# Performance work log

Measured on AMD Instinct MI355X. Metric: run time of the kernel, lower is better.

Reference implementation:

```python
import jax, jax.numpy as jnp
import numpy as np

EMBED_DIM = 384
HIDDEN_DIM = 512
CODEBOOK_SIZE = 256
NUM_QUANTIZERS = 4
COMMIT_WEIGHT = 0.25
BATCH = 65536


def setup_inputs() -> dict:
    key = jax.random.key(0)
    ks = jax.random.split(key, 10)
    s_in = 1.0 / np.sqrt(EMBED_DIM)
    s_h = 1.0 / np.sqrt(HIDDEN_DIM)
    return {
        "x": jax.random.normal(ks[0], (BATCH, EMBED_DIM), jnp.float32),
        "enc_w1": jax.random.uniform(ks[1], (EMBED_DIM, HIDDEN_DIM), jnp.float32, -s_in, s_in),
        "enc_b1": jnp.zeros((HIDDEN_DIM,), jnp.float32),
        "enc_w2": jax.random.uniform(ks[2], (HIDDEN_DIM, HIDDEN_DIM), jnp.float32, -s_h, s_h),
        "enc_b2": jnp.zeros((HIDDEN_DIM,), jnp.float32),
        "codebooks": jax.random.normal(ks[3], (NUM_QUANTIZERS, CODEBOOK_SIZE, HIDDEN_DIM), jnp.float32),
        "dec_w1": jax.random.uniform(ks[4], (HIDDEN_DIM, HIDDEN_DIM), jnp.float32, -s_h, s_h),
        "dec_b1": jnp.zeros((HIDDEN_DIM,), jnp.float32),
        "dec_w2": jax.random.uniform(ks[5], (HIDDEN_DIM, EMBED_DIM), jnp.float32, -s_h, s_h),
        "dec_b2": jnp.zeros((EMBED_DIM,), jnp.float32),
    }


def _residual_vq(z, codebooks):
    """Sequential residual VQ with straight-through estimator and commitment loss.
    z: [B, D]; codebooks: [Q, K, D]. Returns quantized [B, D], indices [B, Q], commit_loss scalar."""
    residual = z
    quantized_out = jnp.zeros_like(z)
    commit_loss = jnp.asarray(0.0, z.dtype)
    idx_list = []
    for q in range(NUM_QUANTIZERS):
        cb = codebooks[q]  # [K, D]
        # nearest code: argmin ||r - c||^2 == argmax (2 r.c - ||c||^2)
        scores = 2.0 * (residual @ cb.T) - jnp.sum(cb * cb, axis=-1)  # [B, K]
        idx = jnp.argmax(scores, axis=-1)  # [B]
        quant = cb[idx]  # [B, D] gather
        commit_loss = commit_loss + COMMIT_WEIGHT * jnp.mean(
            (residual - jax.lax.stop_gradient(quant)) ** 2)
        # straight-through: value = quant, gradient flows to residual
        quant_st = residual + jax.lax.stop_gradient(quant - residual)
        quantized_out = quantized_out + quant_st
        residual = residual - jax.lax.stop_gradient(quant)
        idx_list.append(idx)
    indices = jnp.stack(idx_list, axis=-1)  # [B, Q]
    return quantized_out, indices, commit_loss


def reference(x, enc_w1, enc_b1, enc_w2, enc_b2, codebooks,
              dec_w1, dec_b1, dec_w2, dec_b2):
    # encoder MLP
    z = jax.nn.relu(x @ enc_w1 + enc_b1) @ enc_w2 + enc_b2  # [B, H]
    quantized, indices, commit_loss = _residual_vq(z, codebooks)
    # decoder MLP
    recon = jax.nn.relu(quantized @ dec_w1 + dec_b1) @ dec_w2 + dec_b2  # [B, E]
    recon_loss = jnp.mean((recon - x) ** 2)
    return recon, indices, recon_loss, commit_loss
```

## Files before the change

### kernel.cpp

```cpp
#include <hip/hip_runtime.h>
#include <cfloat>
#include <cstddef>
#include <cstdint>


#define BATCH   65536
#define EDIM    384
#define HDIM    512
#define NCODE   256
#define NQ      4

#define OUT_IDX_OFF 25165824
#define OUT_RL_OFF  25427968
#define WS_P0       0
#define WS_P1       33554432
#define WS_CBW      67108864
#define WS_CNORM    67633152
#define WS_COMMITP  67634176
#define WS_RECONP   67636224
#define WS_W1S      67637760
#define WS_W2S      67834368
#define WS_W3S      68096512
#define WS_W4S      68358656
#define WS_CBA      68555264
#define WS_G6       69079552
#define WS_ZN       69472768
#define WS_SSTAR    69538304
#define WS_IDXI     69800448

typedef _Float16 half8 __attribute__((ext_vector_type(8)));
typedef float    f32x16 __attribute__((ext_vector_type(16)));

__device__ __forceinline__ void cvt_hl8(const float* vs, half8& h, half8& l)
{
#pragma unroll
    for (int j = 0; j < 8; ++j) {
        _Float16 hv = (_Float16)vs[j];
        h[j] = hv;
        l[j] = (_Float16)(vs[j] - (float)hv);
    }
}

__device__ __forceinline__ void gll16(const unsigned short* g, unsigned short* l)
{
    __builtin_amdgcn_global_load_lds(
        (const __attribute__((address_space(1))) unsigned int*)g,
        (__attribute__((address_space(3))) unsigned int*)l, 16, 0, 0);
}

template <int N> __device__ __forceinline__ void waitvm()
{
    __builtin_amdgcn_sched_barrier(0);
    if constexpr (N == 0)      asm volatile("s_waitcnt vmcnt(0)" ::: "memory");
    else if constexpr (N == 2) asm volatile("s_waitcnt vmcnt(2)" ::: "memory");
    else if constexpr (N == 3) asm volatile("s_waitcnt vmcnt(3)" ::: "memory");
    else if constexpr (N == 4) asm volatile("s_waitcnt vmcnt(4)" ::: "memory");
    else if constexpr (N == 6) asm volatile("s_waitcnt vmcnt(6)" ::: "memory");
    __builtin_amdgcn_sched_barrier(0);
}
__device__ __forceinline__ void barrier_raw()
{
    __builtin_amdgcn_s_barrier();
    __builtin_amdgcn_sched_barrier(0);
}

__global__ __launch_bounds__(256)
void split_act(const float* __restrict__ src, unsigned short* __restrict__ dst,
               int K)
{
    int u = blockIdx.x * 256 + threadIdx.x;
    int upr = K >> 3;
    int row = u / upr;
    int rem = u % upr;
    int kt = rem >> 1, kh = rem & 1;
    const float* p = src + (size_t)row * K + kt * 16 + kh * 8;
    float vs[8];
#pragma unroll
    for (int j = 0; j < 8; ++j) vs[j] = p[j];
    half8 h, l;
    cvt_hl8(vs, h, l);
    unsigned short* o = dst + (size_t)row * (2 * K) + kt * 32 + kh * 8;
    *reinterpret_cast<half8*>(o)      = h;
    *reinterpret_cast<half8*>(o + 16) = l;
}

__device__ __forceinline__ void body_split_w(const float* __restrict__ W,
                                             unsigned short* __restrict__ out,
                                             int N, int u)
{
    int col  = u % N;
    int rem  = u / N;
    int kh   = rem & 1;
    int kt   = rem >> 1;
    int kbase = kt * 16 + kh * 8;
    float vs[8];
#pragma unroll
    for (int j = 0; j < 8; ++j) vs[j] = W[(size_t)(kbase + j) * N + col];
    half8 h, l;
    cvt_hl8(vs, h, l);
    *reinterpret_cast<half8*>(out + ((size_t)(kt * 4 + kh) * N + col) * 8)     = h;
    *reinterpret_cast<half8*>(out + ((size_t)(kt * 4 + 2 + kh) * N + col) * 8) = l;
}

__device__ __forceinline__ void body_split_cbw(const float* __restrict__ cb,
                                               unsigned short* __restrict__ out,
                                               int u)
{
    int col = u & 1023;
    int rem = u >> 10;
    int kh = rem & 1;
    int kt = rem >> 1;
    const float* p = cb + (size_t)col * HDIM + kt * 16 + kh * 8;
    float vs[8];
#pragma unroll
    for (int j = 0; j < 8; ++j) vs[j] = p[j];
    half8 h, l;
    cvt_hl8(vs, h, l);
    *reinterpret_cast<half8*>(out + ((size_t)(kt * 4 + kh) * 1024 + col) * 8)     = h;
    *reinterpret_cast<half8*>(out + ((size_t)(kt * 4 + 2 + kh) * 1024 + col) * 8) = l;
}

__device__ __forceinline__ void body_split_cba(const float* __restrict__ cb,
                                               unsigned short* __restrict__ out,
                                               int u)
{
    int row = u >> 6;
    int rem = u & 63;
    int kt = rem >> 1, kh = rem & 1;
    const float* p = cb + (size_t)row * HDIM + kt * 16 + kh * 8;
    float vs[8];
#pragma unroll
    for (int j = 0; j < 8; ++j) vs[j] = p[j];
    half8 h, l;
    cvt_hl8(vs, h, l);
    unsigned short* o = out + (size_t)row * 1024 + kt * 32 + kh * 8;
    *reinterpret_cast<half8*>(o)      = h;
    *reinterpret_cast<half8*>(o + 16) = l;
}

__global__ __launch_bounds__(256)
void split_wall(const float* __restrict__ ew1, const float* __restrict__ ew2,
                const float* __restrict__ dw1, const float* __restrict__ dw2,
                const float* __restrict__ cb,
                unsigned short* __restrict__ w1s, unsigned short* __restrict__ w2s,
                unsigned short* __restrict__ w3s, unsigned short* __restrict__ w4s,
                unsigned short* __restrict__ cbw, unsigned short* __restrict__ cba)
{
    const int b = blockIdx.x, tid = threadIdx.x;
    if (b < 96)        body_split_w(ew1, w1s, HDIM, b * 256 + tid);
    else if (b < 224)  body_split_w(ew2, w2s, HDIM, (b - 96) * 256 + tid);
    else if (b < 352)  body_split_w(dw1, w3s, HDIM, (b - 224) * 256 + tid);
    else if (b < 448)  body_split_w(dw2, w4s, EDIM, (b - 352) * 256 + tid);
    else if (b < 704)  body_split_cbw(cb, cbw, (b - 448) * 256 + tid);
    else               body_split_cba(cb, cba, (b - 704) * 256 + tid);
}

__global__ __launch_bounds__(64)
void cnorm_kernel(const float* __restrict__ cb, float* __restrict__ cnorm)
{
    const int code = blockIdx.x;
    const int lane = threadIdx.x;
    const float* r = cb + (size_t)code * HDIM;
    float s = 0.f;
    for (int k = lane; k < HDIM; k += 64) s = fmaf(r[k], r[k], s);
#pragma unroll
    for (int off = 32; off > 0; off >>= 1) s += __shfl_down(s, off);
    if (lane == 0) cnorm[code] = s;
}

__global__ __launch_bounds__(256)
void rownorm(const unsigned short* __restrict__ zs, float* __restrict__ zn)
{
    const int tid = threadIdx.x, wid = tid >> 6, lane = tid & 63;
    const int row = blockIdx.x * 4 + wid;
    const unsigned short* p = zs + (size_t)row * 1024
                                 + (lane >> 1) * 32 + (lane & 1) * 8;
    half8 h = *reinterpret_cast<const half8*>(p);
    half8 l = *reinterpret_cast<const half8*>(p + 16);
    float s = 0.f;
#pragma unroll
    for (int e = 0; e < 8; ++e) {
        float v = (float)h[e] + (float)l[e];
        s = fmaf(v, v, s);
    }
#pragma unroll
    for (int off = 32; off > 0; off >>= 1) s += __shfl_down(s, off);
    if (lane == 0) zn[row] = s;
}

template <int BN, int NKT, int OMODE, bool RELU, bool S3, bool OUTH>
__global__ __launch_bounds__(512, 2)
void gemm_pl(const unsigned short* __restrict__ Ain,
             const unsigned short* __restrict__ Wsp,
             const float* __restrict__ bias, void* __restrict__ Cout,
             const float* __restrict__ X, float* __restrict__ lossP,
             int N, int ldc)
{
    constexpr int WN  = BN / 64;
    constexpr int WM  = 8 / WN;
    constexpr int MR  = 256 / WM;
    constexpr int FM  = MR / 32;
    constexpr int K   = NKT * 16;
    constexpr int BOFF = S3 ? 8192 : 4096;
    constexpr int BUFU = BOFF + 32 * BN;
    constexpr int GPI  = (S3 ? 2 : 1) + ((BN == 256) ? 2 : 1);

    __shared__ __align__(16) unsigned short lds[3][BUFU];

    const int tid  = threadIdx.x;
    const int wid  = tid >> 6;
    const int lane = tid & 63;
    const int l31  = lane & 31;
    const int lh   = lane >> 5;
    const int wm   = wid / WN;
    const int wn   = wid % WN;

    int row0, n0, bx = 0, by = 0, pair = 0;
    const unsigned short* Abase = Ain;
    if constexpr (OMODE == 3) {
        const int ptab[6] = {0, 0, 0, 1, 1, 2};
        const int qtab[6] = {1, 2, 3, 2, 3, 3};
        pair = blockIdx.x;
        Abase = Ain + (size_t)ptab[pair] * 256 * 1024;
        row0 = 0;
        n0   = qtab[pair] * 256;
    } else {
        int bidx = blockIdx.y * gridDim.x + blockIdx.x;
        const int nwg = gridDim.x * gridDim.y;
        if ((nwg & 7) == 0) {
            const int cpx = nwg >> 3;
            bidx = (bidx & 7) * cpx + (bidx >> 3);
        }
        bx = bidx % gridDim.x;
        by = bidx / gridDim.x;
        row0 = by * 256;
        n0   = bx * BN;
    }

    f32x16 acc[FM][2];
#pragma unroll
    for (int m = 0; m < FM; ++m)
#pragma unroll
        for (int n = 0; n < 2; ++n) acc[m][n] = (f32x16)(0.0f);

    auto stageA = [&](int buf, int kt) {
#pragma unroll
        for (int t = 0; t < (S3 ? 2 : 1); ++t) {
            const int i = t * 8 + wid;
            const int u = i >> 2;
            const int row = (i & 3) * 64 + lane;
            gll16(Abase + (size_t)(row0 + row) * (2 * K) + kt * 32 + u * 8,
                  &lds[buf][(size_t)i * 512 + (size_t)lane * 8]);
        }
    };
    auto stageB = [&](int buf, int kt) {
        const unsigned short* img = Wsp + (size_t)kt * 4 * N * 8;
        unsigned short* dstb = &lds[buf][BOFF];
        if constexpr (BN == 256) {
#pragma unroll
            for (int t = 0; t < 2; ++t) {
                const int i = t * 8 + wid;
                const int u = i >> 2;
                const int col = (i & 3) * 64 + lane;
                gll16(img + ((size_t)u * N + n0 + col) * 8,
                      dstb + (size_t)i * 512 + (size_t)lane * 8);
            }
        } else {
            const int u = wid >> 1;
            const int col = (wid & 1) * 64 + lane;
            gll16(img + ((size_t)u * N + n0 + col) * 8,
                  dstb + (size_t)wid * 512 + (size_t)lane * 8);
        }
    };
    auto compute = [&](int buf) {
        const unsigned short* Ab = &lds[buf][0];
        const unsigned short* Bb = &lds[buf][BOFF];
        half8 Ah[FM], Al[FM];
#pragma unroll
        for (int fm = 0; fm < FM; ++fm) {
            const int row = wm * MR + fm * 32 + l31;
            Ah[fm] = *reinterpret_cast<const half8*>(Ab + ((size_t)lh * 256 + row) * 8);
            if constexpr (S3)
                Al[fm] = *reinterpret_cast<const half8*>(Ab + ((size_t)(2 + lh) * 256 + row) * 8);
        }
#pragma unroll
        for (int nt = 0; nt < 2; ++nt) {
            const int col = wn * 64 + nt * 32 + l31;
            half8 Bh = *reinterpret_cast<const half8*>(Bb + ((size_t)lh * BN + col) * 8);
            half8 Bl = *reinterpret_cast<const half8*>(Bb + ((size_t)(2 + lh) * BN + col) * 8);
#pragma unroll
            for (int fm = 0; fm < FM; ++fm) {
                acc[fm][nt] = __builtin_amdgcn_mfma_f32_32x32x16_f16(Ah[fm], Bh, acc[fm][nt], 0, 0, 0);
                acc[fm][nt] = __builtin_amdgcn_mfma_f32_32x32x16_f16(Ah[fm], Bl, acc[fm][nt], 0, 0, 0);
                if constexpr (S3)
                    acc[fm][nt] = __builtin_amdgcn_mfma_f32_32x32x16_f16(Al[fm], Bh, acc[fm][nt], 0, 0, 0);
            }
        }
    };

    stageA(0, 0); stageB(0, 0);
    stageA(1, 1); stageB(1, 1);
    waitvm<GPI>();
    barrier_raw();
    for (int kt = 0; kt < NKT; ++kt) {
        const int cur = kt % 3;
        if (kt + 2 < NKT) { const int nb = (kt + 2) % 3; stageA(nb, kt + 2); stageB(nb, kt + 2); }
        compute(cur);
        if (kt < NKT - 2) waitvm<GPI>(); else waitvm<0>();
        barrier_raw();
    }

    if constexpr (OMODE == 0) {
        unsigned short* o = (unsigned short*)Cout;
        const size_t rs = (size_t)N * 2;
#pragma unroll
        for (int fm = 0; fm < FM; ++fm) {
#pragma unroll
            for (int nt = 0; nt < 2; ++nt) {
                const int col = n0 + wn * 64 + nt * 32 + l31;
                const float b = bias[col];
                const size_t cbo = (size_t)(col >> 4) * 32 + (size_t)((col >> 3) & 1) * 8 + (col & 7);
#pragma unroll
                for (int rg = 0; rg < 16; ++rg) {
                    const int row = row0 + wm * MR + fm * 32 + (rg & 3) + 8 * (rg >> 2) + 4 * lh;
                    float v = acc[fm][nt][rg] + b;
                    if (RELU) v = v > 0.f ? v : 0.f;
                    _Float16 hv = (_Float16)v;
                    union { _Float16 f; unsigned short u; } ch;
                    ch.f = hv;
                    o[(size_t)row * rs + cbo] = ch.u;
                    if constexpr (!OUTH) {
                        _Float16 lv = (_Float16)(v - (float)hv);
                        union { _Float16 f; unsigned short u; } cl;
                        cl.f = lv;
                        o[(size_t)row * rs + cbo + 16] = cl.u;
                    }
                }
            }
        }
    } else if constexpr (OMODE == 1) {
        float* C = (float*)Cout;
        float lacc = 0.f;
#pragma unroll
        for (int fm = 0; fm < FM; ++fm) {
#pragma unroll
            for (int nt = 0; nt < 2; ++nt) {
                const int col = n0 + wn * 64 + nt * 32 + l31;
                if (col < N) {
                    const float b = bias[col];
#pragma unroll
                    for (int rg = 0; rg < 16; ++rg) {
                        const int row = row0 + wm * MR + fm * 32 + (rg & 3) + 8 * (rg >> 2) + 4 * lh;
                        float v = acc[fm][nt][rg] + b;
                        if (RELU) v = v > 0.f ? v : 0.f;
                        C[(size_t)row * N + col] = v;
                        float d = v - X[(size_t)row * N + col];
                        lacc = fmaf(d, d, lacc);
                    }
                }
            }
        }
        __shared__ float red[512];
        red[tid] = lacc;
        __syncthreads();
        for (int s = 256; s > 0; s >>= 1) {
            if (tid < s) red[tid] += red[tid + s];
            __syncthreads();
        }
        if (tid == 0) lossP[by * gridDim.x + bx] = red[0];
    } else if constexpr (OMODE == 2) {
        float* C = (float*)Cout;
#pragma unroll
        for (int fm = 0; fm < FM; ++fm) {
#pragma unroll
            for (int nt = 0; nt < 2; ++nt) {
                const int col = n0 + wn * 64 + nt * 32 + l31;
#pragma unroll
                for (int rg = 0; rg < 16; ++rg) {
                    const int row = row0 + wm * MR + fm * 32 + (rg & 3) + 8 * (rg >> 2) + 4 * lh;
                    C[(size_t)row * ldc + col] = acc[fm][nt][rg];
                }
            }
        }
    } else {
        float* C = (float*)Cout + (size_t)pair * 65536;
#pragma unroll
        for (int fm = 0; fm < FM; ++fm) {
#pragma unroll
            for (int nt = 0; nt < 2; ++nt) {
                const int colL = wn * 64 + nt * 32 + l31;
#pragma unroll
                for (int rg = 0; rg < 16; ++rg) {
                    const int row = wm * MR + fm * 32 + (rg & 3) + 8 * (rg >> 2) + 4 * lh;
                    C[(size_t)row * 256 + colL] = acc[fm][nt][rg];
                }
            }
        }
    }
}

__global__ __launch_bounds__(256)
void vq_argmax(const float* __restrict__ S,
               const float* __restrict__ G6,
               const float* __restrict__ cnorm,
               float* __restrict__ idx_out,
               int* __restrict__ idxi,
               float* __restrict__ sstar,
               int rowbase)
{
    const int tid = threadIdx.x, wid = tid >> 6, lane = tid & 63;
    const int lrow = blockIdx.x * 4 + wid;
    const int grow = rowbase + lrow;
    const float* srow = S + (size_t)lrow * 1024;
    const int c0 = lane * 4;

    int iprev0 = 0, iprev1 = 0, iprev2 = 0;

#pragma unroll
    for (int q = 0; q < NQ; ++q) {
        float4 sv = *reinterpret_cast<const float4*>(srow + q * 256 + c0);
        float a[4] = {sv.x, sv.y, sv.z, sv.w};
        if (q >= 1) {
            const float* g = G6 + ((size_t)(q - 1) * 256 + iprev0) * 256 + c0;
            float4 gv = *reinterpret_cast<const float4*>(g);
            a[0] -= gv.x; a[1] -= gv.y; a[2] -= gv.z; a[3] -= gv.w;
        }
        if (q >= 2) {
            const float* g = G6 + ((size_t)(q + 1) * 256 + iprev1) * 256 + c0;
            float4 gv = *reinterpret_cast<const float4*>(g);
            a[0] -= gv.x; a[1] -= gv.y; a[2] -= gv.z; a[3] -= gv.w;
        }
        if (q >= 3) {
            const float* g = G6 + ((size_t)5 * 256 + iprev2) * 256 + c0;
            float4 gv = *reinterpret_cast<const float4*>(g);
            a[0] -= gv.x; a[1] -= gv.y; a[2] -= gv.z; a[3] -= gv.w;
        }
        float4 cnv = *reinterpret_cast<const float4*>(cnorm + q * 256 + c0);
        float cna[4] = {cnv.x, cnv.y, cnv.z, cnv.w};

        float bv = -FLT_MAX;
        int   bi = 0;
#pragma unroll
        for (int j = 0; j < 4; ++j) {
            float s = 2.f * a[j] - cna[j];
            const int code = c0 + j;
            if (s > bv || (s == bv && code < bi)) { bv = s; bi = code; }
        }
#pragma unroll
        for (int m = 1; m < 64; m <<= 1) {
            float ov = __shfl_xor(bv, m, 64);
            int   oi = __shfl_xor(bi, m, 64);
            if (ov > bv || (ov == bv && oi < bi)) { bv = ov; bi = oi; }
        }
        if (q == 0) iprev0 = bi;
        else if (q == 1) iprev1 = bi;
        else if (q == 2) iprev2 = bi;
        if (lane == 0) {
            idxi[q * 65536 + grow]  = bi;
            sstar[q * 65536 + grow] = bv;
            idx_out[(size_t)grow * NQ + q] = (float)bi;
        }
    }
}

__global__ __launch_bounds__(256)
void vq_quant(const int* __restrict__ idxi, const float* __restrict__ sstar,
              const float* __restrict__ zn, const float* __restrict__ cb,
              unsigned short* __restrict__ qout, float* __restrict__ commitP)
{
    __shared__ float red[256];
    const int tid = threadIdx.x, wid = tid >> 6, lane = tid & 63;
    float ca = 0.f;

#pragma unroll
    for (int t = 0; t < 8; ++t) {
        const int row = blockIdx.x * 32 + wid * 8 + t;
        const int i0 = idxi[row],          i1 = idxi[65536 + row];
        const int i2 = idxi[131072 + row], i3 = idxi[196608 + row];
        const int koff = lane * 8;
        const float* c0 = cb + ((size_t)(0 * NCODE + i0)) * HDIM + koff;
        const float* c1 = cb + ((size_t)(1 * NCODE + i1)) * HDIM + koff;
        const float* c2 = cb + ((size_t)(2 * NCODE + i2)) * HDIM + koff;
        const float* c3 = cb + ((size_t)(3 * NCODE + i3)) * HDIM + koff;
        float q[8];
#pragma unroll
        for (int hh = 0; hh < 2; ++hh) {
            float4 v0 = *reinterpret_cast<const float4*>(c0 + hh * 4);
            float4 v1 = *reinterpret_cast<const float4*>(c1 + hh * 4);
            float4 v2 = *reinterpret_cast<const float4*>(c2 + hh * 4);
            float4 v3 = *reinterpret_cast<const float4*>(c3 + hh * 4);
            q[hh * 4 + 0] = ((v0.x + v1.x) + v2.x) + v3.x;
            q[hh * 4 + 1] = ((v0.y + v1.y) + v2.y) + v3.y;
            q[hh * 4 + 2] = ((v0.z + v1.z) + v2.z) + v3.z;
            q[hh * 4 + 3] = ((v0.w + v1.w) + v2.w) + v3.w;
        }
        half8 oh;
#pragma unroll
        for (int e = 0; e < 8; ++e) oh[e] = (_Float16)q[e];
        unsigned short* op = qout + (size_t)row * 1024
                                  + (lane >> 1) * 32 + (lane & 1) * 8;
        *reinterpret_cast<half8*>(op) = oh;

        if (lane == 0) {
            float rn = zn[row];
            rn -= sstar[row];           float cm = rn;
            rn -= sstar[65536 + row];   cm += rn;
            rn -= sstar[131072 + row];  cm += rn;
            rn -= sstar[196608 + row];  cm += rn;
            ca += cm;
        }
    }

    red[tid] = ca;
    __syncthreads();
    for (int s = 128; s > 0; s >>= 1) {
        if (tid < s) red[tid] += red[tid + s];
        __syncthreads();
    }
    if (tid == 0) commitP[blockIdx.x] = red[0];
}

__global__ __launch_bounds__(256)
void loss_reduce(const float* __restrict__ cP, int nc,
                 const float* __restrict__ rP, int nr,
                 float* __restrict__ out2)
{
    __shared__ float red[256];
    const int tid = threadIdx.x;

    float s = 0.f;
    for (int i = tid; i < nc; i += 256) s += cP[i];
    red[tid] = s;
    __syncthreads();
    for (int st = 128; st > 0; st >>= 1) {
        if (tid < st) red[tid] += red[tid + st];
        __syncthreads();
    }
    float ctot = red[0];
    __syncthreads();

    s = 0.f;
    for (int i = tid; i < nr; i += 256) s += rP[i];
    red[tid] = s;
    __syncthreads();
    for (int st = 128; st > 0; st >>= 1) {
        if (tid < st) red[tid] += red[tid + st];
        __syncthreads();
    }
    if (tid == 0) {
        out2[0] = red[0] / ((float)BATCH * (float)EDIM);
        out2[1] = 0.25f * ctot / ((float)BATCH * (float)HDIM);
    }
}

extern "C" void kernel_launch(void* const* d_in, const int* in_sizes, int n_in,
                              void* d_out, int out_size, void* d_ws, size_t ws_size,
                              hipStream_t stream)
{
    const float* x   = (const float*)d_in[0];
    const float* ew1 = (const float*)d_in[1];
    const float* eb1 = (const float*)d_in[2];
    const float* ew2 = (const float*)d_in[3];
    const float* eb2 = (const float*)d_in[4];
    const float* cb  = (const float*)d_in[5];
    const float* dw1 = (const float*)d_in[6];
    const float* db1 = (const float*)d_in[7];
    const float* dw2 = (const float*)d_in[8];
    const float* db2 = (const float*)d_in[9];

    float* out = (float*)d_out;
    float* ws  = (float*)d_ws;
    unsigned short* P0  = (unsigned short*)(ws + WS_P0);
    unsigned short* P1  = (unsigned short*)(ws + WS_P1);
    unsigned short* XS  = P1;
    float* Sbuf = ws + WS_P0;
    unsigned short* cbw = (unsigned short*)(ws + WS_CBW);
    unsigned short* cba = (unsigned short*)(ws + WS_CBA);
    float* G6 = ws + WS_G6;
    float* zn = ws + WS_ZN;
    float* ss = ws + WS_SSTAR;
    int*   ii = (int*)(ws + WS_IDXI);
    float* cn = ws + WS_CNORM;
    float* cP = ws + WS_COMMITP;
    float* rP = ws + WS_RECONP;
    unsigned short* w1s = (unsigned short*)(ws + WS_W1S);
    unsigned short* w2s = (unsigned short*)(ws + WS_W2S);
    unsigned short* w3s = (unsigned short*)(ws + WS_W3S);
    unsigned short* w4s = (unsigned short*)(ws + WS_W4S);

    cnorm_kernel<<<NQ * NCODE, 64, 0, stream>>>(cb, cn);
    split_act<<<BATCH * 48 / 256, 256, 0, stream>>>(x, XS, EDIM);
    split_wall<<<960, 256, 0, stream>>>(ew1, ew2, dw1, dw2, cb,
                                        w1s, w2s, w3s, w4s, cbw, cba);

    gemm_pl<256, 32, 3, false, true, false><<<dim3(6, 1), 512, 0, stream>>>(
        cba, cbw, nullptr, G6, nullptr, nullptr, 1024, 256);

    gemm_pl<256, 24, 0, true, true, false><<<dim3(HDIM / 256, BATCH / 256), 512, 0, stream>>>(
        XS, w1s, eb1, P0, nullptr, nullptr, HDIM, HDIM);
    gemm_pl<256, 32, 0, false, true, false><<<dim3(HDIM / 256, BATCH / 256), 512, 0, stream>>>(
        P0, w2s, eb2, P1, nullptr, nullptr, HDIM, HDIM);

    rownorm<<<BATCH / 4, 256, 0, stream>>>(P1, zn);

    float* idxo = out + OUT_IDX_OFF;
    for (int half = 0; half < 2; ++half) {
        const int rowbase = half * 32768;
        gemm_pl<256, 32, 2, false, true, false><<<dim3(4, 128), 512, 0, stream>>>(
            P1 + (size_t)rowbase * 1024, cbw, nullptr, Sbuf,
            nullptr, nullptr, 1024, 1024);
        vq_argmax<<<8192, 256, 0, stream>>>(Sbuf, G6, cn, idxo, ii, ss, rowbase);
    }

    vq_quant<<<BATCH / 32, 256, 0, stream>>>(ii, ss, zn, cb, P0, cP);

    gemm_pl<256, 32, 0, true, false, true><<<dim3(HDIM / 256, BATCH / 256), 512, 0, stream>>>(
        P0, w3s, db1, P1, nullptr, nullptr, HDIM, HDIM);
    gemm_pl<128, 32, 1, false, false, false><<<dim3(EDIM / 128, BATCH / 256), 512, 0, stream>>>(
        P1, w4s, db2, out, x, rP, EDIM, EDIM);

    loss_reduce<<<1, 256, 0, stream>>>(cP, BATCH / 32, rP,
                                       (EDIM / 128) * (BATCH / 256),
                                       out + OUT_RL_OFF);
}
```

Before: 848.8 us.

## Restructure GEMM LDS pipeline to double-buffer two k-tiles per barrier

Replaces the three-stage single-k-tile ring buffer with a two-buffer scheme where each buffer holds two k-tiles. Each iteration prefetches the next pair while computing two k-tiles, then waits on vmcnt(0) and synchronizes, halving the number of barriers per GEMM. The cost is a full wait on outstanding loads each step rather than partial vmcnt waits, and a larger LDS footprint (four tiles instead of three), which may reduce occupancy and lower prefetch depth relative to compute.

```diff
diff --git a/kernel.cpp b/kernel.cpp
--- a/kernel.cpp
+++ b/kernel.cpp
@@ -48,14 +48,10 @@
         (__attribute__((address_space(3))) unsigned int*)l, 16, 0, 0);
 }
 
-template <int N> __device__ __forceinline__ void waitvm()
+__device__ __forceinline__ void waitvm0()
 {
     __builtin_amdgcn_sched_barrier(0);
-    if constexpr (N == 0)      asm volatile("s_waitcnt vmcnt(0)" ::: "memory");
-    else if constexpr (N == 2) asm volatile("s_waitcnt vmcnt(2)" ::: "memory");
-    else if constexpr (N == 3) asm volatile("s_waitcnt vmcnt(3)" ::: "memory");
-    else if constexpr (N == 4) asm volatile("s_waitcnt vmcnt(4)" ::: "memory");
-    else if constexpr (N == 6) asm volatile("s_waitcnt vmcnt(6)" ::: "memory");
+    asm volatile("s_waitcnt vmcnt(0)" ::: "memory");
     __builtin_amdgcn_sched_barrier(0);
 }
 __device__ __forceinline__ void barrier_raw()
@@ -201,11 +197,11 @@
     constexpr int MR  = 256 / WM;
     constexpr int FM  = MR / 32;
     constexpr int K   = NKT * 16;
-    constexpr int BOFF = S3 ? 8192 : 4096;
-    constexpr int BUFU = BOFF + 32 * BN;
-    constexpr int GPI  = (S3 ? 2 : 1) + ((BN == 256) ? 2 : 1);
-
-    __shared__ __align__(16) unsigned short lds[3][BUFU];
+    constexpr int BOFF  = S3 ? 8192 : 4096;
+    constexpr int TILEU = BOFF + 32 * BN;
+    constexpr int NP    = NKT / 2;
+
+    __shared__ __align__(16) unsigned short lds[2][2 * TILEU];
 
     const int tid  = threadIdx.x;
     const int wid  = tid >> 6;
@@ -243,19 +239,20 @@
 #pragma unroll
         for (int n = 0; n < 2; ++n) acc[m][n] = (f32x16)(0.0f);
 
-    auto stageA = [&](int buf, int kt) {
+    auto stageA = [&](int buf, int slot, int kt) {
+        unsigned short* base = &lds[buf][(size_t)slot * TILEU];
 #pragma unroll
         for (int t = 0; t < (S3 ? 2 : 1); ++t) {
             const int i = t * 8 + wid;
             const int u = i >> 2;
             const int row = (i & 3) * 64 + lane;
             gll16(Abase + (size_t)(row0 + row) * (2 * K) + kt * 32 + u * 8,
-                  &lds[buf][(size_t)i * 512 + (size_t)lane * 8]);
+                  base + (size_t)i * 512 + (size_t)lane * 8);
         }
     };
-    auto stageB = [&](int buf, int kt) {
+    auto stageB = [&](int buf, int slot, int kt) {
         const unsigned short* img = Wsp + (size_t)kt * 4 * N * 8;
-        unsigned short* dstb = &lds[buf][BOFF];
+        unsigned short* dstb = &lds[buf][(size_t)slot * TILEU + BOFF];
         if constexpr (BN == 256) {
 #pragma unroll
             for (int t = 0; t < 2; ++t) {
@@ -272,9 +269,9 @@
                   dstb + (size_t)wid * 512 + (size_t)lane * 8);
         }
     };
-    auto compute = [&](int buf) {
-        const unsigned short* Ab = &lds[buf][0];
-        const unsigned short* Bb = &lds[buf][BOFF];
+    auto compute = [&](int buf, int slot) {
+        const unsigned short* Ab = &lds[buf][(size_t)slot * TILEU];
+        const unsigned short* Bb = Ab + BOFF;
         half8 Ah[FM], Al[FM];
 #pragma unroll
         for (int fm = 0; fm < FM; ++fm) {
@@ -298,15 +295,20 @@
         }
     };
 
-    stageA(0, 0); stageB(0, 0);
-    stageA(1, 1); stageB(1, 1);
-    waitvm<GPI>();
+    stageA(0, 0, 0); stageB(0, 0, 0);
+    stageA(0, 1, 1); stageB(0, 1, 1);
+    waitvm0();
     barrier_raw();
-    for (int kt = 0; kt < NKT; ++kt) {
-        const int cur = kt % 3;
-        if (kt + 2 < NKT) { const int nb = (kt + 2) % 3; stageA(nb, kt + 2); stageB(nb, kt + 2); }
-        compute(cur);
-        if (kt < NKT - 2) waitvm<GPI>(); else waitvm<0>();
+    for (int p = 0; p < NP; ++p) {
+        const int cur = p & 1;
+        if (p + 1 < NP) {
+            const int nb = cur ^ 1;
+            stageA(nb, 0, 2 * p + 2); stageB(nb, 0, 2 * p + 2);
+            stageA(nb, 1, 2 * p + 3); stageB(nb, 1, 2 * p + 3);
+        }
+        compute(cur, 0);
+        compute(cur, 1);
+        waitvm0();
         barrier_raw();
     }
 
```

Measured after the change: 876.6 us. 1.03x slower.

## Add phased double-pair LDS pipeline with setprio for BN=256 split-3 GEMM

Applied to the files above, without the earlier changes.

For the BN=256, three-MFMA split-precision GEMM variant, the kernel now uses four LDS tile slots that hold two k-tile pairs at once. The main loop is split into four phases per pair, and the global-to-LDS loads for the next pair are spread across those phases. Explicit barriers and lgkmcnt waits separate the LDS reads from the MFMA bursts, and s_setprio raises wave priority during the MFMA sections. The aim is to overlap memory traffic with MFMA work better and to reduce contention between waves. In exchange, LDS use grows, which may cut occupancy, and each pair now carries more barriers.

```diff
diff --git a/kernel.cpp b/kernel.cpp
--- a/kernel.cpp
+++ b/kernel.cpp
@@ -58,6 +58,11 @@
     else if constexpr (N == 6) asm volatile("s_waitcnt vmcnt(6)" ::: "memory");
     __builtin_amdgcn_sched_barrier(0);
 }
+__device__ __forceinline__ void waitlgkm0()
+{
+    asm volatile("s_waitcnt lgkmcnt(0)" ::: "memory");
+    __builtin_amdgcn_sched_barrier(0);
+}
 __device__ __forceinline__ void barrier_raw()
 {
     __builtin_amdgcn_s_barrier();
@@ -201,11 +206,13 @@
     constexpr int MR  = 256 / WM;
     constexpr int FM  = MR / 32;
     constexpr int K   = NKT * 16;
-    constexpr int BOFF = S3 ? 8192 : 4096;
-    constexpr int BUFU = BOFF + 32 * BN;
+    constexpr int BOFF  = S3 ? 8192 : 4096;
+    constexpr int TILEU = BOFF + 32 * BN;
+    constexpr bool PHASED = (BN == 256) && S3;
+    constexpr int LDSU = PHASED ? 4 * TILEU : 3 * TILEU;
     constexpr int GPI  = (S3 ? 2 : 1) + ((BN == 256) ? 2 : 1);
 
-    __shared__ __align__(16) unsigned short lds[3][BUFU];
+    __shared__ __align__(16) unsigned short lds[LDSU];
 
     const int tid  = threadIdx.x;
     const int wid  = tid >> 6;
@@ -215,15 +222,15 @@
     const int wm   = wid / WN;
     const int wn   = wid % WN;
 
-    int row0, n0, bx = 0, by = 0, pair = 0;
+    int row0, n0, bx = 0, by = 0, pairi = 0;
     const unsigned short* Abase = Ain;
     if constexpr (OMODE == 3) {
         const int ptab[6] = {0, 0, 0, 1, 1, 2};
         const int qtab[6] = {1, 2, 3, 2, 3, 3};
-        pair = blockIdx.x;
-        Abase = Ain + (size_t)ptab[pair] * 256 * 1024;
+        pairi = blockIdx.x;
+        Abase = Ain + (size_t)ptab[pairi] * 256 * 1024;
         row0 = 0;
-        n0   = qtab[pair] * 256;
+        n0   = qtab[pairi] * 256;
     } else {
         int bidx = blockIdx.y * gridDim.x + blockIdx.x;
         const int nwg = gridDim.x * gridDim.y;
@@ -243,19 +250,20 @@
 #pragma unroll
         for (int n = 0; n < 2; ++n) acc[m][n] = (f32x16)(0.0f);
 
-    auto stageA = [&](int buf, int kt) {
+    auto stageA = [&](int slot, int kt) {
+        unsigned short* base = lds + (size_t)slot * TILEU;
 #pragma unroll
         for (int t = 0; t < (S3 ? 2 : 1); ++t) {
             const int i = t * 8 + wid;
             const int u = i >> 2;
             const int row = (i & 3) * 64 + lane;
             gll16(Abase + (size_t)(row0 + row) * (2 * K) + kt * 32 + u * 8,
-                  &lds[buf][(size_t)i * 512 + (size_t)lane * 8]);
+                  base + (size_t)i * 512 + (size_t)lane * 8);
         }
     };
-    auto stageB = [&](int buf, int kt) {
+    auto stageB = [&](int slot, int kt) {
         const unsigned short* img = Wsp + (size_t)kt * 4 * N * 8;
-        unsigned short* dstb = &lds[buf][BOFF];
+        unsigned short* dstb = lds + (size_t)slot * TILEU + BOFF;
         if constexpr (BN == 256) {
 #pragma unroll
             for (int t = 0; t < 2; ++t) {
@@ -272,9 +280,9 @@
                   dstb + (size_t)wid * 512 + (size_t)lane * 8);
         }
     };
-    auto compute = [&](int buf) {
-        const unsigned short* Ab = &lds[buf][0];
-        const unsigned short* Bb = &lds[buf][BOFF];
+    auto compute = [&](int slot) {
+        const unsigned short* Ab = lds + (size_t)slot * TILEU;
+        const unsigned short* Bb = Ab + BOFF;
         half8 Ah[FM], Al[FM];
 #pragma unroll
         for (int fm = 0; fm < FM; ++fm) {
@@ -298,16 +306,67 @@
         }
     };
 
-    stageA(0, 0); stageB(0, 0);
-    stageA(1, 1); stageB(1, 1);
-    waitvm<GPI>();
-    barrier_raw();
-    for (int kt = 0; kt < NKT; ++kt) {
-        const int cur = kt % 3;
-        if (kt + 2 < NKT) { const int nb = (kt + 2) % 3; stageA(nb, kt + 2); stageB(nb, kt + 2); }
-        compute(cur);
-        if (kt < NKT - 2) waitvm<GPI>(); else waitvm<0>();
+    if constexpr (PHASED) {
+        constexpr int NP = NKT / 2;
+        stageA(0, 0); stageB(0, 0);
+        stageA(1, 1); stageB(1, 1);
+        waitvm<0>();
         barrier_raw();
+        for (int pr = 0; pr < NP; ++pr) {
+            const int cb2 = (pr & 1) * 2;
+            const int nb2 = cb2 ^ 2;
+#pragma unroll
+            for (int ph = 0; ph < 4; ++ph) {
+                const int fmh = ph >> 1, nt = ph & 1;
+                const int col = wn * 64 + nt * 32 + l31;
+                half8 Ahf[2][2], Alf[2][2], Bhf[2], Blf[2];
+#pragma unroll
+                for (int s = 0; s < 2; ++s) {
+                    const unsigned short* Ab = lds + (size_t)(cb2 + s) * TILEU;
+                    const unsigned short* Bb = Ab + BOFF;
+#pragma unroll
+                    for (int f = 0; f < 2; ++f) {
+                        const int fm = fmh * 2 + f;
+                        const int row = wm * MR + fm * 32 + l31;
+                        Ahf[s][f] = *reinterpret_cast<const half8*>(Ab + ((size_t)lh * 256 + row) * 8);
+                        Alf[s][f] = *reinterpret_cast<const half8*>(Ab + ((size_t)(2 + lh) * 256 + row) * 8);
+                    }
+                    Bhf[s] = *reinterpret_cast<const half8*>(Bb + ((size_t)lh * BN + col) * 8);
+                    Blf[s] = *reinterpret_cast<const half8*>(Bb + ((size_t)(2 + lh) * BN + col) * 8);
+                }
+                if (pr + 1 < NP) {
+                    if (ph == 0) { stageA(nb2, 2 * pr + 2); stageA(nb2 + 1, 2 * pr + 3); }
+                    else if (ph == 1) { stageB(nb2, 2 * pr + 2); stageB(nb2 + 1, 2 * pr + 3); }
+                }
+                barrier_raw();
+                waitlgkm0();
+                __builtin_amdgcn_s_setprio(1);
+#pragma unroll
+                for (int s = 0; s < 2; ++s)
+#pragma unroll
+                    for (int f = 0; f < 2; ++f) {
+                        const int fm = fmh * 2 + f;
+                        acc[fm][nt] = __builtin_amdgcn_mfma_f32_32x32x16_f16(Ahf[s][f], Bhf[s], acc[fm][nt], 0, 0, 0);
+                        acc[fm][nt] = __builtin_amdgcn_mfma_f32_32x32x16_f16(Ahf[s][f], Blf[s], acc[fm][nt], 0, 0, 0);
+                        acc[fm][nt] = __builtin_amdgcn_mfma_f32_32x32x16_f16(Alf[s][f], Bhf[s], acc[fm][nt], 0, 0, 0);
+                    }
+                __builtin_amdgcn_s_setprio(0);
+                if (ph == 3) waitvm<0>();
+                barrier_raw();
+            }
+        }
+    } else {
+        stageA(0, 0); stageB(0, 0);
+        stageA(1, 1); stageB(1, 1);
+        waitvm<GPI>();
+        barrier_raw();
+        for (int kt = 0; kt < NKT; ++kt) {
+            const int cur = kt % 3;
+            if (kt + 2 < NKT) { const int nb = (kt + 2) % 3; stageA(nb, kt + 2); stageB(nb, kt + 2); }
+            compute(cur);
+            if (kt < NKT - 2) waitvm<GPI>(); else waitvm<0>();
+            barrier_raw();
+        }
     }
 
     if constexpr (OMODE == 0) {
@@ -383,7 +442,7 @@
             }
         }
     } else {
-        float* C = (float*)Cout + (size_t)pair * 65536;
+        float* C = (float*)Cout + (size_t)pairi * 65536;
 #pragma unroll
         for (int fm = 0; fm < FM; ++fm) {
 #pragma unroll
```

After: 894.1 us. +5.3%, slower.
